# Performance work log

Hardware: AMD Instinct MI355X
Metric: run time of the kernel (lower is better)

Reference implementation:

```python
import jax, jax.numpy as jnp
import numpy as np

C = 256          # num_channel
CE = C // 4      # encoded channels = 64
T = 16           # seq_len
K = 7            # filter_size
D = 1            # dilation
G = 4            # num_groups
PAD = ((K - 1) * D) // 2  # 3
K2G = K * K * G  # 196
EPS = 1e-5


def _bn(x, gamma, beta, mean, var):
    # inference-mode BatchNorm3d over channel axis 1
    inv = gamma * jax.lax.rsqrt(var + EPS)
    return x * inv[None, :, None, None, None] + (beta - mean * inv)[None, :, None, None, None]


def _conv1x1(x, w):
    # x: (B, Cin, T, H, W), w: (Cout, Cin) -> (B, Cout, T, H, W)
    return jnp.einsum('bcthw,oc->bothw', x, w)


def _correlation(x, filter_weight):
    # x: (B, CE, T, H, W); filter_weight: (CE, T, K, K)
    B, c, t, h, w = x.shape
    # x1: temporal shift (repeat first frame)
    x1 = jnp.concatenate([x[:, :, :1], x[:, :, :-1]], axis=2)
    x2 = jnp.pad(x, ((0, 0), (0, 0), (0, 0), (PAD, PAD), (PAD, PAD)))
    outs = []
    for ky in range(K):          # dy outer (torch meshgrid 'ij' order)
        for kx in range(K):
            dy, dx = ky * D, kx * D
            wgt = filter_weight[:, :, ky, kx]  # (CE, T)
            r = wgt[None, :, :, None, None] * x1 * x2[:, :, :, dy:dy + h, dx:dx + w]
            r = r.reshape(B, G, c // G, t, h, w).mean(axis=2)  # (B, G, T, H, W)
            outs.append(r)
    return jnp.concatenate(outs, axis=1)  # (B, K^2*G, T, H, W)


def setup_inputs() -> dict:
    key = jax.random.key(0)
    ks = jax.random.split(key, 12)
    B, H, W = 4, 56, 56
    inp = {
        'x': jax.random.normal(ks[0], (B, C, T, H, W), jnp.float32),
        'enc_w': jax.random.normal(ks[1], (CE, C), jnp.float32) * (2.0 / C) ** 0.5,
        'enc_gamma': jax.random.uniform(ks[2], (CE,), jnp.float32, 0.5, 1.5),
        'enc_beta': jax.random.normal(ks[3], (CE,), jnp.float32) * 0.1,
        'enc_mean': jax.random.normal(ks[4], (CE,), jnp.float32) * 0.1,
        'enc_var': jax.random.uniform(ks[5], (CE,), jnp.float32, 0.5, 1.5),
        'filter_weight': jax.random.normal(ks[6], (CE, T, K, K), jnp.float32) * (2.0 / (T * K * K)) ** 0.5,
        'dec_w': jax.random.normal(ks[7], (C, K2G), jnp.float32) * (2.0 / K2G) ** 0.5,
        'dec_gamma': jax.random.uniform(ks[8], (C,), jnp.float32, 0.5, 1.5),
        'dec_beta': jax.random.normal(ks[9], (C,), jnp.float32) * 0.1,
        'dec_mean': jax.random.normal(ks[10], (C,), jnp.float32) * 0.1,
        'dec_var': jax.random.uniform(ks[11], (C,), jnp.float32, 0.5, 1.5),
    }
    return inp


def reference(x, enc_w, enc_gamma, enc_beta, enc_mean, enc_var,
              filter_weight, dec_w, dec_gamma, dec_beta, dec_mean, dec_var):
    x_enc = jax.nn.relu(_bn(_conv1x1(x, enc_w), enc_gamma, enc_beta, enc_mean, enc_var))
    x_corr = _correlation(x_enc, filter_weight)
    x_dec = _bn(_conv1x1(x_corr, dec_w), dec_gamma, dec_beta, dec_mean, dec_var)
    return jax.nn.relu(x + x_dec)
```

## Files before the change

### kernel.cpp

```cpp
#include <hip/hip_runtime.h>

#define CC   256
#define CEE  64
#define TT   16
#define KKK  7
#define PADK 3
#define GGG  4
#define CGP  16
#define K2G  196
#define KPAD 224
#define HHH  56
#define WWW  56
#define HW   3136
#define THW  50176
#define BBB  4

typedef _Float16 f16x8 __attribute__((ext_vector_type(8)));
typedef float    f32x4 __attribute__((ext_vector_type(4)));

#define N_XENC   (BBB*CEE*THW)
#define OFF_XENC 0
#define OFF_EWT  (N_XENC)
#define OFF_ESC  (OFF_EWT + CC*CEE)
#define OFF_ESH  (OFF_ESC + CEE)
#define OFF_DWTH (OFF_ESH + CEE)
#define OFF_DSC  (OFF_DWTH + (CC*KPAD)/2)
#define OFF_DSH  (OFF_DSC + CC)

__global__ void prep_kernel(const float* __restrict__ enc_w,
                            const float* __restrict__ eg, const float* __restrict__ eb,
                            const float* __restrict__ em, const float* __restrict__ ev,
                            const float* __restrict__ dec_w,
                            const float* __restrict__ dg, const float* __restrict__ db,
                            const float* __restrict__ dm, const float* __restrict__ dv,
                            float* __restrict__ ewt, float* __restrict__ esc, float* __restrict__ esh,
                            _Float16* __restrict__ dwth, float* __restrict__ dsc, float* __restrict__ dsh) {
    int i = blockIdx.x * blockDim.x + threadIdx.x;
    int n = blockDim.x * gridDim.x;
    for (int idx = i; idx < CC * CEE; idx += n) {
        int c = idx >> 6, o = idx & 63;
        ewt[idx] = enc_w[o * CC + c];
    }
    for (int idx = i; idx < CC * KPAD; idx += n) {
        int o = idx / KPAD;
        int k = idx - o * KPAD;
        int ky = k >> 5, rem = k & 31, gg = rem >> 3, kx = rem & 7;
        float v = 0.f;
        if (kx < 7) v = dec_w[o * K2G + (ky * 7 + kx) * GGG + gg];
        dwth[idx] = (_Float16)v;
    }
    for (int idx = i; idx < CEE; idx += n) {
        float inv = eg[idx] * rsqrtf(ev[idx] + 1e-5f);
        esc[idx] = inv;
        esh[idx] = eb[idx] - em[idx] * inv;
    }
    for (int idx = i; idx < CC; idx += n) {
        float inv = dg[idx] * rsqrtf(dv[idx] + 1e-5f);
        dsc[idx] = inv;
        dsh[idx] = db[idx] - dm[idx] * inv;
    }
}

__global__ void __launch_bounds__(256) enc_kernel(
        const float* __restrict__ x, const float* __restrict__ ewt,
        const float* __restrict__ esc, const float* __restrict__ esh,
        float* __restrict__ xenc) {
    __shared__ float wlds[64 * 64];
    const int tid  = threadIdx.x;
    const int og   = tid >> 6;
    const int lane = tid & 63;
    const int b    = blockIdx.x / 196;
    const int q0   = (blockIdx.x % 196) * 256 + lane * 4;
    const float* xb = x + (size_t)b * CC * THW + q0;

    f32x4 acc[16];
    #pragma unroll
    for (int i = 0; i < 16; ++i) acc[i] = (f32x4){0.f, 0.f, 0.f, 0.f};

    #pragma unroll 1
    for (int chunk = 0; chunk < 4; ++chunk) {
        __syncthreads();
        const float4* src = (const float4*)(ewt + chunk * 4096);
        float4* dst = (float4*)wlds;
        #pragma unroll
        for (int k = 0; k < 4; ++k) dst[k * 256 + tid] = src[k * 256 + tid];
        __syncthreads();

        f32x4 xv[4];
        #pragma unroll
        for (int u = 0; u < 4; ++u)
            xv[u] = *(const f32x4*)(xb + (size_t)(chunk * 64 + u) * THW);

        #pragma unroll 1
        for (int cb = 0; cb < 16; ++cb) {
            f32x4 xvn[4];
            if (cb < 15) {
                #pragma unroll
                for (int u = 0; u < 4; ++u)
                    xvn[u] = *(const f32x4*)(xb + (size_t)(chunk * 64 + (cb + 1) * 4 + u) * THW);
            }
            #pragma unroll
            for (int u = 0; u < 4; ++u) {
                const f32x4* wr = (const f32x4*)(wlds + (cb * 4 + u) * 64 + og * 16);
                #pragma unroll
                for (int oi4 = 0; oi4 < 4; ++oi4) {
                    f32x4 w4 = wr[oi4];
                    acc[oi4 * 4 + 0] += w4[0] * xv[u];
                    acc[oi4 * 4 + 1] += w4[1] * xv[u];
                    acc[oi4 * 4 + 2] += w4[2] * xv[u];
                    acc[oi4 * 4 + 3] += w4[3] * xv[u];
                }
            }
            if (cb < 15) {
                #pragma unroll
                for (int u = 0; u < 4; ++u) xv[u] = xvn[u];
            }
        }
    }

    const size_t outbase = (size_t)b * CEE * THW + q0;
    #pragma unroll
    for (int oi = 0; oi < 16; ++oi) {
        const int o = og * 16 + oi;
        const float sc = esc[o];
        const float sh = esh[o];
        f32x4 v = acc[oi] * sc + sh;
        #pragma unroll
        for (int r = 0; r < 4; ++r) v[r] = v[r] > 0.f ? v[r] : 0.f;
        *(f32x4*)(xenc + outbase + (size_t)o * THW) = v;
    }
}

__global__ void __launch_bounds__(256, 3) corr_dec_kernel(
        const float* __restrict__ x, const float* __restrict__ xenc,
        const float* __restrict__ fw, const _Float16* __restrict__ dwth,
        const float* __restrict__ dsc, const float* __restrict__ dsh,
        float* __restrict__ out) {
    __shared__ _Float16 x2t[64 * 14 * 16];
    __shared__ float wg[64 * 49];
    __shared__ __align__(16) _Float16 corr_h[64 * 40];

    const int tid = threadIdx.x;
    const int g = tid >> 6;
    const int lane = tid & 63;
    const int ph = lane >> 3;
    const int pw = lane & 7;

    const int bx = blockIdx.x;
    const int tile = bx % 49;
    const int t = (bx / 49) & 15;
    const int b = bx / 784;
    const int th0 = (tile / 7) * 8;
    const int tw0 = (tile % 7) * 8;

    for (int i = tid; i < 64 * 224; i += 256) {
        int c = i / 224;
        int rem = i - c * 224;
        int hy = rem >> 4;
        int hx = rem & 15;
        int h = th0 + hy - PADK;
        int w = tw0 + hx - PADK;
        float v = 0.f;
        if (hx < 14 && (unsigned)h < HHH && (unsigned)w < WWW)
            v = xenc[((b * CEE + c) * TT + t) * HW + h * WWW + w];
        x2t[i] = (_Float16)v;
    }
    for (int i = tid; i < 64 * 49; i += 256) {
        int c = i / 49;
        int o = i - c * 49;
        wg[i] = fw[c * (TT * 49) + t * 49 + o] * (1.f / 16.f);
    }
    const int tprev = t > 0 ? t - 1 : 0;
    const int hwp = (th0 + ph) * WWW + (tw0 + pw);
    float x1r[16];
    #pragma unroll
    for (int j = 0; j < 16; ++j)
        x1r[j] = xenc[((b * CEE + g * CGP + j) * TT + tprev) * HW + hwp];

    f32x4 acc[4][4];
    #pragma unroll
    for (int mi = 0; mi < 4; ++mi)
        #pragma unroll
        for (int ni = 0; ni < 4; ++ni)
            acc[mi][ni] = (f32x4){0.f, 0.f, 0.f, 0.f};

    const int r16 = lane & 15;
    const int quad = lane >> 4;

    __syncthreads();

    #pragma unroll 1
    for (int ky = 0; ky < 7; ++ky) {
        float a[7];
        #pragma unroll
        for (int kx = 0; kx < 7; ++kx) a[kx] = 0.f;
        #pragma unroll
        for (int j = 0; j < 16; ++j) {
            const float x1v = x1r[j];
            const int crow = g * CGP + j;
            const _Float16* x2p = &x2t[(crow * 14 + (ph + ky)) * 16 + pw];
            const float* wrow = &wg[crow * 49 + ky * 7];
            #pragma unroll
            for (int kx = 0; kx < 7; ++kx)
                a[kx] += wrow[kx] * (x1v * (float)x2p[kx]);
        }
        f16x8 pk;
        #pragma unroll
        for (int kx = 0; kx < 7; ++kx) pk[kx] = (_Float16)a[kx];
        pk[7] = (_Float16)0.f;
        *(f16x8*)(corr_h + lane * 40 + g * 8) = pk;

        f16x8 af[4];
        #pragma unroll
        for (int mi = 0; mi < 4; ++mi)
            af[mi] = *(const f16x8*)(dwth + (size_t)(g * 64 + mi * 16 + r16) * KPAD
                                     + ky * 32 + quad * 8);

        __syncthreads();

        f16x8 bf[4];
        #pragma unroll
        for (int ni = 0; ni < 4; ++ni)
            bf[ni] = *(const f16x8*)(corr_h + (ni * 16 + r16) * 40 + quad * 8);
        #pragma unroll
        for (int mi = 0; mi < 4; ++mi)
            #pragma unroll
            for (int ni = 0; ni < 4; ++ni)
                acc[mi][ni] = __builtin_amdgcn_mfma_f32_16x16x32_f16(af[mi], bf[ni],
                                                                     acc[mi][ni], 0, 0, 0);
        __syncthreads();
    }

    #pragma unroll
    for (int mi = 0; mi < 4; ++mi) {
        #pragma unroll
        for (int reg = 0; reg < 4; ++reg) {
            const int o = g * 64 + mi * 16 + quad * 4 + reg;
            const float sc = dsc[o];
            const float sh = dsh[o];
            const int obase = ((b * CC + o) * TT + t) * HW;
            #pragma unroll
            for (int ni = 0; ni < 4; ++ni) {
                const int p = ni * 16 + r16;
                const int idx = obase + (th0 + (p >> 3)) * WWW + tw0 + (p & 7);
                float v = acc[mi][ni][reg] * sc + sh;
                float rr = x[idx] + v;
                out[idx] = rr > 0.f ? rr : 0.f;
            }
        }
    }
}

extern "C" void kernel_launch(void* const* d_in, const int* in_sizes, int n_in,
                              void* d_out, int out_size, void* d_ws, size_t ws_size,
                              hipStream_t stream) {
    const float* x     = (const float*)d_in[0];
    const float* enc_w = (const float*)d_in[1];
    const float* eg    = (const float*)d_in[2];
    const float* eb    = (const float*)d_in[3];
    const float* em    = (const float*)d_in[4];
    const float* ev    = (const float*)d_in[5];
    const float* fw    = (const float*)d_in[6];
    const float* dec_w = (const float*)d_in[7];
    const float* dg    = (const float*)d_in[8];
    const float* db    = (const float*)d_in[9];
    const float* dm    = (const float*)d_in[10];
    const float* dv    = (const float*)d_in[11];
    float* out = (float*)d_out;
    float* ws  = (float*)d_ws;

    prep_kernel<<<104, 256, 0, stream>>>(enc_w, eg, eb, em, ev, dec_w, dg, db, dm, dv,
                                         ws + OFF_EWT, ws + OFF_ESC, ws + OFF_ESH,
                                         (_Float16*)(ws + OFF_DWTH),
                                         ws + OFF_DSC, ws + OFF_DSH);
    enc_kernel<<<784, 256, 0, stream>>>(x, ws + OFF_EWT, ws + OFF_ESC, ws + OFF_ESH,
                                        ws + OFF_XENC);
    corr_dec_kernel<<<3136, 256, 0, stream>>>(x, ws + OFF_XENC, fw,
                                              (const _Float16*)(ws + OFF_DWTH),
                                              ws + OFF_DSC, ws + OFF_DSH,
                                              out);
}
```

Baseline: 849.3 us.

## Halve enc tile width, store filter weights as fp16, raise occupancy bounds

The encoder kernel now gives each thread two spatial outputs instead of four and launches twice as many blocks, with a launch bound of 4 blocks per CU. Filter weights are pre-scaled and converted to fp16 in the prep kernel, which halves the LDS they use in the correlation kernel. That kernel's occupancy bound rises from 3 to 4 blocks, and the decoder-weight fragment loads are hoisted to the top of each ky iteration. The aims are lower register and LDS pressure for more waves in flight and earlier issue of the global loads. In exchange, the encoder reloads the LDS weights for half as many outputs per block, and fp16 filter weights reduce precision.

```diff
diff --git a/kernel.cpp b/kernel.cpp
--- a/kernel.cpp
+++ b/kernel.cpp
@@ -17,6 +17,7 @@
 
 typedef _Float16 f16x8 __attribute__((ext_vector_type(8)));
 typedef float    f32x4 __attribute__((ext_vector_type(4)));
+typedef float    f32x2 __attribute__((ext_vector_type(2)));
 
 #define N_XENC   (BBB*CEE*THW)
 #define OFF_XENC 0
@@ -26,15 +27,18 @@
 #define OFF_DWTH (OFF_ESH + CEE)
 #define OFF_DSC  (OFF_DWTH + (CC*KPAD)/2)
 #define OFF_DSH  (OFF_DSC + CC)
+#define OFF_FWH  (OFF_DSH + CC)
 
 __global__ void prep_kernel(const float* __restrict__ enc_w,
                             const float* __restrict__ eg, const float* __restrict__ eb,
                             const float* __restrict__ em, const float* __restrict__ ev,
+                            const float* __restrict__ fw,
                             const float* __restrict__ dec_w,
                             const float* __restrict__ dg, const float* __restrict__ db,
                             const float* __restrict__ dm, const float* __restrict__ dv,
                             float* __restrict__ ewt, float* __restrict__ esc, float* __restrict__ esh,
-                            _Float16* __restrict__ dwth, float* __restrict__ dsc, float* __restrict__ dsh) {
+                            _Float16* __restrict__ dwth, float* __restrict__ dsc, float* __restrict__ dsh,
+                            _Float16* __restrict__ fwh) {
     int i = blockIdx.x * blockDim.x + threadIdx.x;
     int n = blockDim.x * gridDim.x;
     for (int idx = i; idx < CC * CEE; idx += n) {
@@ -49,6 +53,9 @@
         if (kx < 7) v = dec_w[o * K2G + (ky * 7 + kx) * GGG + gg];
         dwth[idx] = (_Float16)v;
     }
+    for (int idx = i; idx < CEE * TT * 49; idx += n) {
+        fwh[idx] = (_Float16)(fw[idx] * (1.f / 16.f));
+    }
     for (int idx = i; idx < CEE; idx += n) {
         float inv = eg[idx] * rsqrtf(ev[idx] + 1e-5f);
         esc[idx] = inv;
@@ -61,7 +68,7 @@
     }
 }
 
-__global__ void __launch_bounds__(256) enc_kernel(
+__global__ void __launch_bounds__(256, 4) enc_kernel(
         const float* __restrict__ x, const float* __restrict__ ewt,
         const float* __restrict__ esc, const float* __restrict__ esh,
         float* __restrict__ xenc) {
@@ -69,13 +76,13 @@
     const int tid  = threadIdx.x;
     const int og   = tid >> 6;
     const int lane = tid & 63;
-    const int b    = blockIdx.x / 196;
-    const int q0   = (blockIdx.x % 196) * 256 + lane * 4;
+    const int b    = blockIdx.x / 392;
+    const int q0   = (blockIdx.x % 392) * 128 + lane * 2;
     const float* xb = x + (size_t)b * CC * THW + q0;
 
-    f32x4 acc[16];
-    #pragma unroll
-    for (int i = 0; i < 16; ++i) acc[i] = (f32x4){0.f, 0.f, 0.f, 0.f};
+    f32x2 acc[16];
+    #pragma unroll
+    for (int i = 0; i < 16; ++i) acc[i] = (f32x2){0.f, 0.f};
 
     #pragma unroll 1
     for (int chunk = 0; chunk < 4; ++chunk) {
@@ -86,18 +93,18 @@
         for (int k = 0; k < 4; ++k) dst[k * 256 + tid] = src[k * 256 + tid];
         __syncthreads();
 
-        f32x4 xv[4];
+        f32x2 xv[4];
         #pragma unroll
         for (int u = 0; u < 4; ++u)
-            xv[u] = *(const f32x4*)(xb + (size_t)(chunk * 64 + u) * THW);
+            xv[u] = *(const f32x2*)(xb + (size_t)(chunk * 64 + u) * THW);
 
         #pragma unroll 1
         for (int cb = 0; cb < 16; ++cb) {
-            f32x4 xvn[4];
+            f32x2 xvn[4];
             if (cb < 15) {
                 #pragma unroll
                 for (int u = 0; u < 4; ++u)
-                    xvn[u] = *(const f32x4*)(xb + (size_t)(chunk * 64 + (cb + 1) * 4 + u) * THW);
+                    xvn[u] = *(const f32x2*)(xb + (size_t)(chunk * 64 + (cb + 1) * 4 + u) * THW);
             }
             #pragma unroll
             for (int u = 0; u < 4; ++u) {
@@ -124,20 +131,20 @@
         const int o = og * 16 + oi;
         const float sc = esc[o];
         const float sh = esh[o];
-        f32x4 v = acc[oi] * sc + sh;
-        #pragma unroll
-        for (int r = 0; r < 4; ++r) v[r] = v[r] > 0.f ? v[r] : 0.f;
-        *(f32x4*)(xenc + outbase + (size_t)o * THW) = v;
-    }
-}
-
-__global__ void __launch_bounds__(256, 3) corr_dec_kernel(
+        f32x2 v = acc[oi] * sc + sh;
+        v[0] = v[0] > 0.f ? v[0] : 0.f;
+        v[1] = v[1] > 0.f ? v[1] : 0.f;
+        *(f32x2*)(xenc + outbase + (size_t)o * THW) = v;
+    }
+}
+
+__global__ void __launch_bounds__(256, 4) corr_dec_kernel(
         const float* __restrict__ x, const float* __restrict__ xenc,
-        const float* __restrict__ fw, const _Float16* __restrict__ dwth,
+        const _Float16* __restrict__ fwh, const _Float16* __restrict__ dwth,
         const float* __restrict__ dsc, const float* __restrict__ dsh,
         float* __restrict__ out) {
     __shared__ _Float16 x2t[64 * 14 * 16];
-    __shared__ float wg[64 * 49];
+    __shared__ _Float16 wg[64 * 49];
     __shared__ __align__(16) _Float16 corr_h[64 * 40];
 
     const int tid = threadIdx.x;
@@ -168,7 +175,7 @@
     for (int i = tid; i < 64 * 49; i += 256) {
         int c = i / 49;
         int o = i - c * 49;
-        wg[i] = fw[c * (TT * 49) + t * 49 + o] * (1.f / 16.f);
+        wg[i] = fwh[c * (TT * 49) + t * 49 + o];
     }
     const int tprev = t > 0 ? t - 1 : 0;
     const int hwp = (th0 + ph) * WWW + (tw0 + pw);
@@ -191,6 +198,12 @@
 
     #pragma unroll 1
     for (int ky = 0; ky < 7; ++ky) {
+        f16x8 af[4];
+        #pragma unroll
+        for (int mi = 0; mi < 4; ++mi)
+            af[mi] = *(const f16x8*)(dwth + (size_t)(g * 64 + mi * 16 + r16) * KPAD
+                                     + ky * 32 + quad * 8);
+
         float a[7];
         #pragma unroll
         for (int kx = 0; kx < 7; ++kx) a[kx] = 0.f;
@@ -199,22 +212,16 @@
             const float x1v = x1r[j];
             const int crow = g * CGP + j;
             const _Float16* x2p = &x2t[(crow * 14 + (ph + ky)) * 16 + pw];
-            const float* wrow = &wg[crow * 49 + ky * 7];
+            const _Float16* wrow = &wg[crow * 49 + ky * 7];
             #pragma unroll
             for (int kx = 0; kx < 7; ++kx)
-                a[kx] += wrow[kx] * (x1v * (float)x2p[kx]);
+                a[kx] += (float)wrow[kx] * (x1v * (float)x2p[kx]);
         }
         f16x8 pk;
         #pragma unroll
         for (int kx = 0; kx < 7; ++kx) pk[kx] = (_Float16)a[kx];
         pk[7] = (_Float16)0.f;
         *(f16x8*)(corr_h + lane * 40 + g * 8) = pk;
-
-        f16x8 af[4];
-        #pragma unroll
-        for (int mi = 0; mi < 4; ++mi)
-            af[mi] = *(const f16x8*)(dwth + (size_t)(g * 64 + mi * 16 + r16) * KPAD
-                                     + ky * 32 + quad * 8);
 
         __syncthreads();
 
@@ -269,13 +276,15 @@
     float* out = (float*)d_out;
     float* ws  = (float*)d_ws;
 
-    prep_kernel<<<104, 256, 0, stream>>>(enc_w, eg, eb, em, ev, dec_w, dg, db, dm, dv,
+    prep_kernel<<<104, 256, 0, stream>>>(enc_w, eg, eb, em, ev, fw, dec_w, dg, db, dm, dv,
                                          ws + OFF_EWT, ws + OFF_ESC, ws + OFF_ESH,
                                          (_Float16*)(ws + OFF_DWTH),
-                                         ws + OFF_DSC, ws + OFF_DSH);
-    enc_kernel<<<784, 256, 0, stream>>>(x, ws + OFF_EWT, ws + OFF_ESC, ws + OFF_ESH,
-                                        ws + OFF_XENC);
-    corr_dec_kernel<<<3136, 256, 0, stream>>>(x, ws + OFF_XENC, fw,
+                                         ws + OFF_DSC, ws + OFF_DSH,
+                                         (_Float16*)(ws + OFF_FWH));
+    enc_kernel<<<1568, 256, 0, stream>>>(x, ws + OFF_EWT, ws + OFF_ESC, ws + OFF_ESH,
+                                         ws + OFF_XENC);
+    corr_dec_kernel<<<3136, 256, 0, stream>>>(x, ws + OFF_XENC,
+                                              (const _Float16*)(ws + OFF_FWH),
                                               (const _Float16*)(ws + OFF_DWTH),
                                               ws + OFF_DSC, ws + OFF_DSH,
                                               out);
```

After: 919.5 us. +8.3%, slower.
